# Kernel tuning notes

Measured on AMD Instinct MI355X. Metric: run time of the kernel, lower is better.

The kernel has to match this reference:

```python
import jax, jax.numpy as jnp
import numpy as np

N_NODES = 100000
N_EDGES = 3200000
N_FEAT = 128
HIDDEN = 16


def gcn_conv(x, W, b, row, col, ew, n):
    """PyG GCNConv: linear -> add self-loops -> sym deg-norm -> scatter-add -> bias."""
    x = x @ W  # [n, out]
    loop = jnp.arange(n)
    row = jnp.concatenate([row, loop])
    col = jnp.concatenate([col, loop])
    ew = jnp.concatenate([ew, jnp.ones((n,), ew.dtype)])  # self-loop weight 1
    deg = jax.ops.segment_sum(ew, col, num_segments=n)  # in-degree by edge weight
    dinv = jnp.where(deg > 0, jax.lax.rsqrt(deg), 0.0)
    norm = dinv[row] * ew * dinv[col]  # [E+n]
    # gather source features, scale, scatter-add at destinations
    out = jax.ops.segment_sum(x[row] * norm[:, None], col, num_segments=n)
    return out + b


def setup_inputs() -> dict:
    key = jax.random.key(0)
    k = jax.random.split(key, 7)
    x = jax.random.normal(k[0], (N_NODES, N_FEAT), dtype=jnp.float32)
    edge_index = jax.random.randint(k[1], (2, N_EDGES), 0, N_NODES, dtype=jnp.int64)
    edge_weight = jax.random.uniform(k[2], (N_EDGES,), dtype=jnp.float32)
    s1 = 1.0 / np.sqrt(N_FEAT)
    s2 = 1.0 / np.sqrt(HIDDEN)
    W1 = jax.random.uniform(k[3], (N_FEAT, HIDDEN), jnp.float32, -s1, s1)
    b1 = jnp.zeros((HIDDEN,), jnp.float32)
    W2 = jax.random.uniform(k[4], (HIDDEN, 1), jnp.float32, -s2, s2)
    b2 = jnp.zeros((1,), jnp.float32)
    return {"x": x, "edge_index": edge_index, "edge_weight": edge_weight,
            "W1": W1, "b1": b1, "W2": W2, "b2": b2}


def reference(x, edge_index, edge_weight, W1, b1, W2, b2):
    n = x.shape[0]
    row, col = edge_index[0], edge_index[1]
    h = gcn_conv(x, W1, b1, row, col, edge_weight, n)
    h = jax.nn.relu(h)
    h = gcn_conv(h, W2, b2, row, col, edge_weight, n)
    return jax.nn.sigmoid(h)[:, 0].astype(jnp.float32)  # squeeze(1)
```

## Files before the change

### kernel.cpp

```cpp
#include <hip/hip_runtime.h>
#include <hip/hip_fp16.h>
#include <math.h>

#define NNODES 100000
#define NEDGES 3200000
#define NF 128
#define NH 16
#define SB 192
#define NSB 521
#define NBLK 512
#define EPB (NEDGES / NBLK)
#define CAP2 6912
#define XWBLK 391

__device__ __forceinline__ __half2 u2h(unsigned u) { union { unsigned u; __half2 h; } c; c.u = u; return c.h; }
__device__ __forceinline__ unsigned h2u(__half2 h) { union { unsigned u; __half2 h; } c; c.h = h; return c.u; }
__device__ __forceinline__ __half2 shfl_h2(__half2 v, int m) {
    int x = __shfl_xor(*(int*)&v, m);
    return *(__half2*)&x;
}

__global__ void k_histxw(const int* __restrict__ col, unsigned* __restrict__ ghist,
                         const float* __restrict__ x, const float* __restrict__ W1,
                         float* __restrict__ xw) {
    __shared__ float w[NF * NH];
    __shared__ unsigned h[NSB];
    int t = threadIdx.x, b = blockIdx.x;
    if (b < NBLK) {
        for (int i = t; i < NSB; i += 256) h[i] = 0u;
        __syncthreads();
        const int2* c2 = (const int2*)(col + b * EPB);
        for (int i = t; i < EPB / 2; i += 256) {
            int2 c = c2[i];
            atomicAdd(&h[(unsigned)c.x / SB], 1u);
            atomicAdd(&h[(unsigned)c.y / SB], 1u);
        }
        __syncthreads();
        for (int i = t; i < NSB; i += 256) ghist[(size_t)b * NSB + i] = h[i];
    } else {
        for (int i = t; i < NF * NH; i += 256) w[i] = W1[i];
        __syncthreads();
        int i = (b - NBLK) * 256 + t;
        if (i >= NNODES) return;
        float acc[NH];
#pragma unroll
        for (int f = 0; f < NH; ++f) acc[f] = 0.f;
        const float4* xr = (const float4*)(x + (long long)i * NF);
#pragma unroll 8
        for (int k4 = 0; k4 < NF / 4; ++k4) {
            float4 v = xr[k4];
            const float* wk = &w[k4 * 4 * NH];
#pragma unroll
            for (int f = 0; f < NH; ++f)
                acc[f] += v.x * wk[f] + v.y * wk[NH + f] + v.z * wk[2 * NH + f] + v.w * wk[3 * NH + f];
        }
        float4* o = (float4*)(xw + (size_t)i * NH);
#pragma unroll
        for (int q = 0; q < 4; ++q)
            o[q] = make_float4(acc[4 * q], acc[4 * q + 1], acc[4 * q + 2], acc[4 * q + 3]);
    }
}

__global__ __launch_bounds__(NBLK) void k_scan1(unsigned* __restrict__ ghist,
                                                unsigned* __restrict__ totals) {
    int k = blockIdx.x, t = threadIdx.x;
    __shared__ unsigned s[NBLK];
    unsigned v = ghist[(size_t)t * NSB + k];
    s[t] = v;
    __syncthreads();
    for (int off = 1; off < NBLK; off <<= 1) {
        unsigned x = (t >= off) ? s[t - off] : 0u;
        __syncthreads();
        s[t] += x;
        __syncthreads();
    }
    ghist[(size_t)t * NSB + k] = s[t] - v;
    if (t == NBLK - 1) totals[k] = s[t];
}

__global__ void k_scan2(const unsigned* __restrict__ totals, unsigned* __restrict__ sbase,
                        unsigned* __restrict__ start) {
    int t = threadIdx.x;
    __shared__ unsigned s[256];
    unsigned v[3];
    unsigned p = 0;
#pragma unroll
    for (int j = 0; j < 3; ++j) {
        int i = t * 3 + j;
        v[j] = (i < NSB) ? totals[i] : 0u;
        p += v[j];
    }
    s[t] = p;
    __syncthreads();
    for (int off = 1; off < 256; off <<= 1) {
        unsigned x = (t >= off) ? s[t - off] : 0u;
        __syncthreads();
        s[t] += x;
        __syncthreads();
    }
    unsigned run = s[t] - p;
#pragma unroll
    for (int j = 0; j < 3; ++j) {
        int i = t * 3 + j;
        if (i < NSB) sbase[i] = run;
        run += v[j];
    }
    if (t == 255) { sbase[NSB] = NEDGES; start[NNODES] = NEDGES; }
}

__global__ __launch_bounds__(256) void k_scatB1(
        const int* __restrict__ row, const int* __restrict__ col,
        const float* __restrict__ ew,
        const unsigned* __restrict__ ghist, const unsigned* __restrict__ sbase,
        uint2* __restrict__ spack) {
    __shared__ uint2 stage[EPB];
    __shared__ unsigned short sbArr[EPB];
    __shared__ unsigned lcnt[NSB];
    __shared__ unsigned gdelta[NSB];
    __shared__ unsigned scn[256];
    int t = threadIdx.x, b = blockIdx.x;
    int e0 = b * EPB;
    for (int i = t; i < NSB; i += 256) lcnt[i] = 0u;
    __syncthreads();
    const int2* c2 = (const int2*)(col + e0);
    for (int i = t; i < EPB / 2; i += 256) {
        int2 c = c2[i];
        atomicAdd(&lcnt[(unsigned)c.x / SB], 1u);
        atomicAdd(&lcnt[(unsigned)c.y / SB], 1u);
    }
    __syncthreads();
    unsigned v[3];
    unsigned p = 0;
#pragma unroll
    for (int j = 0; j < 3; ++j) {
        int i = t * 3 + j;
        v[j] = (i < NSB) ? lcnt[i] : 0u;
        p += v[j];
    }
    scn[t] = p;
    __syncthreads();
    for (int off = 1; off < 256; off <<= 1) {
        unsigned x = (t >= off) ? scn[t - off] : 0u;
        __syncthreads();
        scn[t] += x;
        __syncthreads();
    }
    unsigned run = scn[t] - p;
    __syncthreads();
    unsigned lst[3];
#pragma unroll
    for (int j = 0; j < 3; ++j) {
        int i = t * 3 + j;
        if (i < NSB) {
            lst[j] = run;
            gdelta[i] = sbase[i] + ghist[(size_t)b * NSB + i] - run;
        }
        run += v[j];
    }
    __syncthreads();
#pragma unroll
    for (int j = 0; j < 3; ++j) {
        int i = t * 3 + j;
        if (i < NSB) lcnt[i] = lst[j];
    }
    __syncthreads();
    const int2* r2 = (const int2*)(row + e0);
    const float2* w2 = (const float2*)(ew + e0);
    for (int i = t; i < EPB / 2; i += 256) {
        int2 rr = r2[i];
        int2 cc = c2[i];
        float2 ww = w2[i];
        unsigned sb = (unsigned)cc.x / SB;
        unsigned ln = (unsigned)cc.x - sb * SB;
        unsigned pos = atomicAdd(&lcnt[sb], 1u);
        stage[pos] = make_uint2((unsigned)rr.x | (ln << 17), __float_as_uint(ww.x));
        sbArr[pos] = (unsigned short)sb;
        sb = (unsigned)cc.y / SB;
        ln = (unsigned)cc.y - sb * SB;
        pos = atomicAdd(&lcnt[sb], 1u);
        stage[pos] = make_uint2((unsigned)rr.y | (ln << 17), __float_as_uint(ww.y));
        sbArr[pos] = (unsigned short)sb;
    }
    __syncthreads();
    for (int i = t; i < EPB; i += 256)
        spack[i + gdelta[sbArr[i]]] = stage[i];
}

__global__ __launch_bounds__(512) void k_sortB2(uint2* __restrict__ spack,
                                                const unsigned* __restrict__ sbase,
                                                unsigned* __restrict__ start,
                                                float* __restrict__ dinv,
                                                const float* __restrict__ xw,
                                                unsigned* __restrict__ xwn) {
    __shared__ uint2 ed[CAP2];
    __shared__ unsigned hist[SB];
    __shared__ float wdeg[SB];
    __shared__ unsigned scn[512];
    int k = blockIdx.x, t = threadIdx.x;
    unsigned e0 = sbase[k], e1 = sbase[k + 1];
    int ne = (int)(e1 - e0);
    if (t < SB) { hist[t] = 0u; wdeg[t] = 0.f; }
    __syncthreads();
    for (int i = t; i < ne; i += 512) {
        uint2 p = spack[e0 + i];
        unsigned ln = p.x >> 17;
        atomicAdd(&hist[ln], 1u);
        atomicAdd(&wdeg[ln], __uint_as_float(p.y));
    }
    __syncthreads();
    unsigned v = (t < SB) ? hist[t] : 0u;
    scn[t] = v;
    __syncthreads();
    for (int off = 1; off < 512; off <<= 1) {
        unsigned x = (t >= off) ? scn[t - off] : 0u;
        __syncthreads();
        scn[t] += x;
        __syncthreads();
    }
    unsigned excl = scn[t] - v;
    int g = k * SB + t;
    float di = 0.f;
    if (t < SB && g < NNODES) {
        start[g] = e0 + excl;
        di = rsqrtf(wdeg[t] + 1.0f);
        dinv[g] = di;
    }
    __syncthreads();
    if (t < SB) hist[t] = excl;
    __syncthreads();
    for (int i = t; i < ne; i += 512) {
        uint2 p = spack[e0 + i];
        unsigned ln = p.x >> 17;
        unsigned pos = atomicAdd(&hist[ln], 1u);
        __half2 hw = __float2half2_rn(__uint_as_float(p.y));
        ed[pos] = make_uint2(p.x & 0x1FFFF, h2u(hw));
    }
    __syncthreads();
    for (int i = t; i < ne; i += 512)
        spack[e0 + i] = ed[i];
    if (t < SB && g < NNODES) {
        const float4* xr = (const float4*)(xw + (size_t)g * NH);
        float4 A = xr[0], B = xr[1], C = xr[2], D = xr[3];
        uint4 o0, o1;
        o0.x = h2u(__floats2half2_rn(A.x * di, A.y * di));
        o0.y = h2u(__floats2half2_rn(A.z * di, A.w * di));
        o0.z = h2u(__floats2half2_rn(B.x * di, B.y * di));
        o0.w = h2u(__floats2half2_rn(B.z * di, B.w * di));
        o1.x = h2u(__floats2half2_rn(C.x * di, C.y * di));
        o1.y = h2u(__floats2half2_rn(C.z * di, C.w * di));
        o1.z = h2u(__floats2half2_rn(D.x * di, D.y * di));
        o1.w = h2u(__floats2half2_rn(D.z * di, D.w * di));
        uint4* o = (uint4*)(xwn + (size_t)g * 8);
        o[0] = o0;
        o[1] = o1;
    }
}

__global__ __launch_bounds__(256) void k_edge1z(
        const uint2* __restrict__ spack, const unsigned* __restrict__ start,
        const unsigned* __restrict__ xwn, const float* __restrict__ dinv,
        const float* __restrict__ b1, const float* __restrict__ W2,
        float* __restrict__ zn) {
    int t = threadIdx.x;
    int n = blockIdx.x * 4 + (t >> 6);
    int lane = t & 63;
    int fg = lane & 3, e4 = lane >> 2;
    unsigned e0 = start[n], e1 = start[n + 1];
    __half2 a0 = __float2half2_rn(0.f), a1 = a0;
    for (unsigned e = e0 + e4; e < e1; e += 48) {
        unsigned ea = e + 16, eb = e + 32;
        uint2 p0 = spack[e];
        uint2 p1 = spack[ea];
        uint2 p2 = spack[eb];
        bool va = ea < e1, vb = eb < e1;
        unsigned r0 = p0.x;
        unsigned r1 = va ? (p1.x & 0x1FFFFu) : r0; if (r1 >= NNODES) r1 = r0;
        unsigned r2 = vb ? (p2.x & 0x1FFFFu) : r0; if (r2 >= NNODES) r2 = r0;
        unsigned w0 = p0.y;
        unsigned w1 = va ? p1.y : 0u;
        unsigned w2 = vb ? p2.y : 0u;
        uint2 q0 = *(const uint2*)(xwn + (size_t)r0 * 8 + fg * 2);
        uint2 q1 = *(const uint2*)(xwn + (size_t)r1 * 8 + fg * 2);
        uint2 q2 = *(const uint2*)(xwn + (size_t)r2 * 8 + fg * 2);
        a0 = __hfma2(u2h(q0.x), u2h(w0), a0);
        a1 = __hfma2(u2h(q0.y), u2h(w0), a1);
        a0 = __hfma2(u2h(q1.x), u2h(w1), a0);
        a1 = __hfma2(u2h(q1.y), u2h(w1), a1);
        a0 = __hfma2(u2h(q2.x), u2h(w2), a0);
        a1 = __hfma2(u2h(q2.y), u2h(w2), a1);
    }
#pragma unroll
    for (int m = 4; m < 64; m <<= 1) {
        a0 = __hadd2(a0, shfl_h2(a0, m));
        a1 = __hadd2(a1, shfl_h2(a1, m));
    }
    float ax = __low2float(a0), ay = __high2float(a0);
    float az = __low2float(a1), aw = __high2float(a1);
    uint2 qs = *(const uint2*)(xwn + (size_t)n * 8 + fg * 2);
    ax += __low2float(u2h(qs.x)); ay += __high2float(u2h(qs.x));
    az += __low2float(u2h(qs.y)); aw += __high2float(u2h(qs.y));
    float di = dinv[n];
    float4 b4 = ((const float4*)b1)[fg];
    float4 w4 = ((const float4*)W2)[fg];
    float s = fmaxf(di * ax + b4.x, 0.f) * w4.x
            + fmaxf(di * ay + b4.y, 0.f) * w4.y
            + fmaxf(di * az + b4.z, 0.f) * w4.z
            + fmaxf(di * aw + b4.w, 0.f) * w4.w;
    s += __shfl_xor(s, 1);
    s += __shfl_xor(s, 2);
    if (lane == 0) zn[n] = s * di;
}

__global__ __launch_bounds__(256) void k_edge2out(
        const uint2* __restrict__ spack, const unsigned* __restrict__ start,
        const float* __restrict__ zn, const float* __restrict__ dinv,
        const float* __restrict__ b2, float* __restrict__ out) {
    int t = threadIdx.x;
    int n = blockIdx.x * 4 + (t >> 6);
    int lane = t & 63;
    unsigned e0 = start[n], e1 = start[n + 1];
    float acc = 0.f;
    for (unsigned e = e0 + lane; e < e1; e += 64) {
        uint2 p = spack[e];
        acc += zn[p.x] * __low2float(u2h(p.y));
    }
#pragma unroll
    for (int m = 1; m < 64; m <<= 1) acc += __shfl_xor(acc, m);
    if (lane == 0) {
        float di = dinv[n];
        float v = di * acc + di * zn[n] + b2[0];
        out[n] = 1.f / (1.f + expf(-v));
    }
}

extern "C" void kernel_launch(void* const* d_in, const int* in_sizes, int n_in,
                              void* d_out, int out_size, void* d_ws, size_t ws_size,
                              hipStream_t stream) {
    const float* x  = (const float*)d_in[0];
    const int* eidx = (const int*)d_in[1];
    const float* ew = (const float*)d_in[2];
    const float* W1 = (const float*)d_in[3];
    const float* b1 = (const float*)d_in[4];
    const float* W2 = (const float*)d_in[5];
    const float* b2 = (const float*)d_in[6];
    float* out = (float*)d_out;

    const int* row = eidx;
    const int* col = eidx + NEDGES;

    unsigned* ws = (unsigned*)d_ws;
    uint2*    spack  = (uint2*)ws;
    float*    xw     = (float*)(ws + 6400000);
    unsigned* xwn    = ws + 8000000;
    float*    dinv   = (float*)(ws + 8800000);
    float*    zn     = (float*)(ws + 8900000);
    unsigned* start  = ws + 9000000;
    unsigned* sbase  = ws + 9100001;
    unsigned* totals = ws + 9100523;
    unsigned* ghist  = ws + 9101044;

    k_histxw <<<NBLK + XWBLK, 256, 0, stream>>>(col, ghist, x, W1, xw);
    k_scan1  <<<NSB, NBLK, 0, stream>>>(ghist, totals);
    k_scan2  <<<1, 256, 0, stream>>>(totals, sbase, start);
    k_scatB1 <<<NBLK, 256, 0, stream>>>(row, col, ew, ghist, sbase, spack);
    k_sortB2 <<<NSB, 512, 0, stream>>>(spack, sbase, start, dinv, xw, xwn);
    k_edge1z <<<NNODES / 4, 256, 0, stream>>>(spack, start, xwn, dinv, b1, W2, zn);
    k_edge2out<<<NNODES / 4, 256, 0, stream>>>(spack, start, zn, dinv, b2, out);
}
```

Measured before the change: 148.6 us.

## Fuse local counting sort with layer-1 aggregation, reading edges from shared memory

The final per-bucket sort and write-back of edges moves out of the degree/dinv kernel into a new 1024-thread kernel. That kernel sorts each bucket's edges into shared memory and then runs the layer-1 gather-aggregate straight from shared memory. The goal is to avoid re-reading the sorted edge array from global memory in the layer-1 pass and to drop the 25k-block launch. The cost is that the degree kernel reads spack twice in a separate launch, and aggregation now uses one wave per 12 nodes with less memory-level parallelism per wave.

```diff
diff --git a/kernel.cpp b/kernel.cpp
--- a/kernel.cpp
+++ b/kernel.cpp
@@ -186,13 +186,10 @@
         spack[i + gdelta[sbArr[i]]] = stage[i];
 }
 
-__global__ __launch_bounds__(512) void k_sortB2(uint2* __restrict__ spack,
-                                                const unsigned* __restrict__ sbase,
-                                                unsigned* __restrict__ start,
-                                                float* __restrict__ dinv,
-                                                const float* __restrict__ xw,
-                                                unsigned* __restrict__ xwn) {
-    __shared__ uint2 ed[CAP2];
+__global__ __launch_bounds__(512) void k_degdinv(
+        const uint2* __restrict__ spack, const unsigned* __restrict__ sbase,
+        unsigned* __restrict__ start, float* __restrict__ dinv,
+        const float* __restrict__ xw, unsigned* __restrict__ xwn) {
     __shared__ unsigned hist[SB];
     __shared__ float wdeg[SB];
     __shared__ unsigned scn[512];
@@ -219,26 +216,10 @@
     }
     unsigned excl = scn[t] - v;
     int g = k * SB + t;
-    float di = 0.f;
     if (t < SB && g < NNODES) {
         start[g] = e0 + excl;
-        di = rsqrtf(wdeg[t] + 1.0f);
+        float di = rsqrtf(wdeg[t] + 1.0f);
         dinv[g] = di;
-    }
-    __syncthreads();
-    if (t < SB) hist[t] = excl;
-    __syncthreads();
-    for (int i = t; i < ne; i += 512) {
-        uint2 p = spack[e0 + i];
-        unsigned ln = p.x >> 17;
-        unsigned pos = atomicAdd(&hist[ln], 1u);
-        __half2 hw = __float2half2_rn(__uint_as_float(p.y));
-        ed[pos] = make_uint2(p.x & 0x1FFFF, h2u(hw));
-    }
-    __syncthreads();
-    for (int i = t; i < ne; i += 512)
-        spack[e0 + i] = ed[i];
-    if (t < SB && g < NNODES) {
         const float4* xr = (const float4*)(xw + (size_t)g * NH);
         float4 A = xr[0], B = xr[1], C = xr[2], D = xr[3];
         uint4 o0, o1;
@@ -256,59 +237,68 @@
     }
 }
 
-__global__ __launch_bounds__(256) void k_edge1z(
-        const uint2* __restrict__ spack, const unsigned* __restrict__ start,
-        const unsigned* __restrict__ xwn, const float* __restrict__ dinv,
-        const float* __restrict__ b1, const float* __restrict__ W2,
-        float* __restrict__ zn) {
-    int t = threadIdx.x;
-    int n = blockIdx.x * 4 + (t >> 6);
-    int lane = t & 63;
+__global__ __launch_bounds__(1024) void k_sedge1(
+        uint2* __restrict__ spack, const unsigned* __restrict__ sbase,
+        const unsigned* __restrict__ start, const unsigned* __restrict__ xwn,
+        const float* __restrict__ dinv, const float* __restrict__ b1,
+        const float* __restrict__ W2, float* __restrict__ zn) {
+    __shared__ uint2 ed[CAP2];
+    __shared__ unsigned lcnt[SB];
+    int k = blockIdx.x, t = threadIdx.x;
+    unsigned e0 = sbase[k], e1 = sbase[k + 1];
+    int ne = (int)(e1 - e0);
+    if (t < SB) {
+        int g = k * SB + t;
+        lcnt[t] = (g < NNODES) ? (start[g] - e0) : (unsigned)ne;
+    }
+    __syncthreads();
+    for (int i = t; i < ne; i += 1024) {
+        uint2 p = spack[e0 + i];
+        unsigned ln = p.x >> 17;
+        unsigned pos = atomicAdd(&lcnt[ln], 1u);
+        __half2 hw = __float2half2_rn(__uint_as_float(p.y));
+        ed[pos] = make_uint2(p.x & 0x1FFFFu, h2u(hw));
+    }
+    __syncthreads();
+    for (int i = t; i < ne; i += 1024)
+        spack[e0 + i] = ed[i];
+    int wave = t >> 6, lane = t & 63;
     int fg = lane & 3, e4 = lane >> 2;
-    unsigned e0 = start[n], e1 = start[n + 1];
-    __half2 a0 = __float2half2_rn(0.f), a1 = a0;
-    for (unsigned e = e0 + e4; e < e1; e += 48) {
-        unsigned ea = e + 16, eb = e + 32;
-        uint2 p0 = spack[e];
-        uint2 p1 = spack[ea];
-        uint2 p2 = spack[eb];
-        bool va = ea < e1, vb = eb < e1;
-        unsigned r0 = p0.x;
-        unsigned r1 = va ? (p1.x & 0x1FFFFu) : r0; if (r1 >= NNODES) r1 = r0;
-        unsigned r2 = vb ? (p2.x & 0x1FFFFu) : r0; if (r2 >= NNODES) r2 = r0;
-        unsigned w0 = p0.y;
-        unsigned w1 = va ? p1.y : 0u;
-        unsigned w2 = vb ? p2.y : 0u;
-        uint2 q0 = *(const uint2*)(xwn + (size_t)r0 * 8 + fg * 2);
-        uint2 q1 = *(const uint2*)(xwn + (size_t)r1 * 8 + fg * 2);
-        uint2 q2 = *(const uint2*)(xwn + (size_t)r2 * 8 + fg * 2);
-        a0 = __hfma2(u2h(q0.x), u2h(w0), a0);
-        a1 = __hfma2(u2h(q0.y), u2h(w0), a1);
-        a0 = __hfma2(u2h(q1.x), u2h(w1), a0);
-        a1 = __hfma2(u2h(q1.y), u2h(w1), a1);
-        a0 = __hfma2(u2h(q2.x), u2h(w2), a0);
-        a1 = __hfma2(u2h(q2.y), u2h(w2), a1);
-    }
-#pragma unroll
-    for (int m = 4; m < 64; m <<= 1) {
-        a0 = __hadd2(a0, shfl_h2(a0, m));
-        a1 = __hadd2(a1, shfl_h2(a1, m));
-    }
-    float ax = __low2float(a0), ay = __high2float(a0);
-    float az = __low2float(a1), aw = __high2float(a1);
-    uint2 qs = *(const uint2*)(xwn + (size_t)n * 8 + fg * 2);
-    ax += __low2float(u2h(qs.x)); ay += __high2float(u2h(qs.x));
-    az += __low2float(u2h(qs.y)); aw += __high2float(u2h(qs.y));
-    float di = dinv[n];
-    float4 b4 = ((const float4*)b1)[fg];
-    float4 w4 = ((const float4*)W2)[fg];
-    float s = fmaxf(di * ax + b4.x, 0.f) * w4.x
-            + fmaxf(di * ay + b4.y, 0.f) * w4.y
-            + fmaxf(di * az + b4.z, 0.f) * w4.z
-            + fmaxf(di * aw + b4.w, 0.f) * w4.w;
-    s += __shfl_xor(s, 1);
-    s += __shfl_xor(s, 2);
-    if (lane == 0) zn[n] = s * di;
+#pragma unroll
+    for (int j = 0; j < SB / 16; ++j) {
+        int ln = wave * (SB / 16) + j;
+        int g = k * SB + ln;
+        if (g >= NNODES) break;
+        unsigned o0 = (ln == 0) ? 0u : lcnt[ln - 1];
+        unsigned o1 = lcnt[ln];
+        __half2 a0 = __float2half2_rn(0.f), a1 = a0;
+        for (unsigned e = o0 + e4; e < o1; e += 16) {
+            uint2 d = ed[e];
+            uint2 q = *(const uint2*)(xwn + (size_t)d.x * 8 + fg * 2);
+            a0 = __hfma2(u2h(q.x), u2h(d.y), a0);
+            a1 = __hfma2(u2h(q.y), u2h(d.y), a1);
+        }
+#pragma unroll
+        for (int m = 4; m < 64; m <<= 1) {
+            a0 = __hadd2(a0, shfl_h2(a0, m));
+            a1 = __hadd2(a1, shfl_h2(a1, m));
+        }
+        float ax = __low2float(a0), ay = __high2float(a0);
+        float az = __low2float(a1), aw = __high2float(a1);
+        uint2 qs = *(const uint2*)(xwn + (size_t)g * 8 + fg * 2);
+        ax += __low2float(u2h(qs.x)); ay += __high2float(u2h(qs.x));
+        az += __low2float(u2h(qs.y)); aw += __high2float(u2h(qs.y));
+        float di = dinv[g];
+        float4 b4 = ((const float4*)b1)[fg];
+        float4 w4 = ((const float4*)W2)[fg];
+        float s = fmaxf(di * ax + b4.x, 0.f) * w4.x
+                + fmaxf(di * ay + b4.y, 0.f) * w4.y
+                + fmaxf(di * az + b4.z, 0.f) * w4.z
+                + fmaxf(di * aw + b4.w, 0.f) * w4.w;
+        s += __shfl_xor(s, 1);
+        s += __shfl_xor(s, 2);
+        if (lane == 0) zn[g] = s * di;
+    }
 }
 
 __global__ __launch_bounds__(256) void k_edge2out(
@@ -363,7 +353,7 @@
     k_scan1  <<<NSB, NBLK, 0, stream>>>(ghist, totals);
     k_scan2  <<<1, 256, 0, stream>>>(totals, sbase, start);
     k_scatB1 <<<NBLK, 256, 0, stream>>>(row, col, ew, ghist, sbase, spack);
-    k_sortB2 <<<NSB, 512, 0, stream>>>(spack, sbase, start, dinv, xw, xwn);
-    k_edge1z <<<NNODES / 4, 256, 0, stream>>>(spack, start, xwn, dinv, b1, W2, zn);
+    k_degdinv<<<NSB, 512, 0, stream>>>(spack, sbase, start, dinv, xw, xwn);
+    k_sedge1 <<<NSB, 1024, 0, stream>>>(spack, sbase, start, xwn, dinv, b1, W2, zn);
     k_edge2out<<<NNODES / 4, 256, 0, stream>>>(spack, start, zn, dinv, b2, out);
 }
```

After: 141.6 us. 4.7% less time.
